# Kernel optimization log

Hardware: AMD Instinct MI355X
Metric: run time of the kernel (lower is better)

## Reference

```python
import jax, jax.numpy as jnp
import numpy as np

N = 1_000_000
C = 32
DIMS = (480, 360, 32)  # cylindrical voxel grid (z/rho, phi, height)
EPS = 1e-5


def setup_inputs() -> dict:
    rng = np.random.default_rng(0)
    total = DIMS[0] * DIMS[1] * DIMS[2]
    # unique active voxels, sorted so searchsorted gives row indices directly
    ids = np.sort(rng.choice(total, size=N, replace=False)).astype(np.int64)
    z = ids // (DIMS[1] * DIMS[2])
    rem = ids % (DIMS[1] * DIMS[2])
    y = rem // DIMS[2]
    x = rem % DIMS[2]
    coords = np.stack([z, y, x], axis=1)
    strides = np.array([DIMS[1] * DIMS[2], DIMS[2], 1], dtype=np.int64)

    def nbr(delta):
        out = np.full((3, N), -1, dtype=np.int32)
        for a in range(3):
            tgt = ids + delta * strides[a]
            ok = (coords[:, a] + delta >= 0) & (coords[:, a] + delta < DIMS[a])
            pos = np.searchsorted(ids, tgt)
            pos_c = np.clip(pos, 0, N - 1)
            found = ok & (ids[pos_c] == tgt)
            out[a] = np.where(found, pos_c, -1).astype(np.int32)
        return out

    nbr_prev = nbr(-1)
    nbr_next = nbr(+1)

    key = jax.random.key(0)
    k0, k1, k2 = jax.random.split(key, 3)
    features = jax.random.normal(k0, (N, C), dtype=jnp.float32)
    # W[branch, tap, in, out]; taps ordered (-1, 0, +1) along the branch's axis
    W = jax.random.normal(k1, (3, 3, C, C), dtype=jnp.float32) * (1.0 / np.sqrt(3 * C))
    gamma = jnp.ones((3, C), dtype=jnp.float32)
    beta = jnp.zeros((3, C), dtype=jnp.float32)
    mean = jax.random.normal(k2, (3, C), dtype=jnp.float32) * 0.1
    var = jnp.ones((3, C), dtype=jnp.float32)
    return {
        "features": features,
        "nbr_prev": jnp.asarray(nbr_prev),
        "nbr_next": jnp.asarray(nbr_next),
        "W": W,
        "gamma": gamma,
        "beta": beta,
        "mean": mean,
        "var": var,
    }


def _branch(f, Wb, prev, nxt, g, b, m, v):
    # 3-tap submanifold conv along one axis: gather prev/next active neighbors
    pm = prev >= 0
    nm = nxt >= 0
    fp = jnp.where(pm[:, None], f[jnp.where(pm, prev, 0)], 0.0)
    fn = jnp.where(nm[:, None], f[jnp.where(nm, nxt, 0)], 0.0)
    out = fp @ Wb[0] + f @ Wb[1] + fn @ Wb[2]
    # BatchNorm1d (inference stats) + Sigmoid
    out = (out - m) * (g * jax.lax.rsqrt(v + EPS)) + b
    return jax.nn.sigmoid(out)


def reference(features, nbr_prev, nbr_next, W, gamma, beta, mean, var):
    acc = jnp.zeros_like(features)
    for a in range(3):  # conv3x1x1, conv1x3x1, conv1x1x3
        acc = acc + _branch(features, W[a], nbr_prev[a], nbr_next[a],
                            gamma[a], beta[a], mean[a], var[a])
    return acc * features  # sparse_add then gating with input features
```

## Files before the change

### kernel.cpp

```cpp
#include <hip/hip_runtime.h>
#include <hip/hip_bf16.h>
#include <stdint.h>


typedef __attribute__((ext_vector_type(8))) __bf16 bf16x8;
typedef __attribute__((ext_vector_type(8))) unsigned short u16x8;
typedef __attribute__((ext_vector_type(4))) float f32x4;
typedef __attribute__((ext_vector_type(2))) float f32x2;

constexpr int NVOX    = 1000000;
constexpr int NTILES  = NVOX / 16;
constexpr int TPW     = 8;
constexpr int WPB     = 4;
constexpr int NWAVES  = (NTILES + TPW - 1) / TPW;
constexpr int NBLOCKS = (NWAVES + WPB - 1) / WPB;

__device__ __forceinline__ unsigned short f2bf_rn(float f) {
    union { float f; unsigned int u; } c; c.f = f;
    return (unsigned short)((c.u + 0x8000u) >> 16);
}

__device__ __forceinline__ bf16x8 cvt_frag(f32x4 lo, f32x4 hi) {
    u16x8 r;
    #pragma unroll
    for (int i = 0; i < 4; ++i) {
        r[i]     = f2bf_rn(lo[i]);
        r[i + 4] = f2bf_rn(hi[i]);
    }
    return __builtin_bit_cast(bf16x8, r);
}

__global__ __launch_bounds__(256) void recon_kernel(
    const float* __restrict__ feat,
    const int*   __restrict__ nprev,
    const int*   __restrict__ nnext,
    const float* __restrict__ Wt,
    const float* __restrict__ gma,
    const float* __restrict__ bta,
    const float* __restrict__ mea,
    const float* __restrict__ var,
    float*       __restrict__ out)
{
    const int lane = threadIdx.x & 63;
    const int n    = lane & 15;
    const int quad = lane >> 4;

    int b   = blockIdx.x;
    int per = NBLOCKS / 8;
    int bs  = (b < per * 8) ? ((b & 7) * per + (b >> 3)) : b;
    int wv  = bs * WPB + (threadIdx.x >> 6);

    const int t0 = wv * TPW;
    if (t0 >= NTILES) return;

    bf16x8 Bf[3][3][2];
    #pragma unroll
    for (int br = 0; br < 3; ++br)
        #pragma unroll
        for (int t = 0; t < 3; ++t)
            #pragma unroll
            for (int h = 0; h < 2; ++h) {
                u16x8 tmp;
                #pragma unroll
                for (int j = 0; j < 8; ++j) {
                    int k = quad * 8 + j;
                    tmp[j] = f2bf_rn(Wt[((br * 3 + t) * 32 + k) * 32 + 2 * n + h]);
                }
                Bf[br][t][h] = __builtin_bit_cast(bf16x8, tmp);
            }

    float sc[3][2], mn[3][2], bt[3][2];
    #pragma unroll
    for (int br = 0; br < 3; ++br)
        #pragma unroll
        for (int h = 0; h < 2; ++h) {
            int c = 2 * n + h;
            float g = gma[br * 32 + c];
            float v = var[br * 32 + c];
            sc[br][h] = g * __frsqrt_rn(v + 1e-5f);
            mn[br][h] = mea[br * 32 + c];
            bt[br][h] = bta[br * 32 + c];
        }

    int ip[3], inx[3];
    {
        int row0 = t0 * 16 + n;
        #pragma unroll
        for (int a = 0; a < 3; ++a) {
            ip[a]  = nprev[a * NVOX + row0];
            inx[a] = nnext[a * NVOX + row0];
        }
    }

    #pragma unroll 1
    for (int tt = 0; tt < TPW; ++tt) {
        int tile = t0 + tt;
        if (tile >= NTILES) return;
        int base = tile * 16;
        int row  = base + n;

        const f32x4* ps = (const f32x4*)(feat + row * 32 + quad * 8);
        f32x4 s_lo = ps[0], s_hi = ps[1];
        f32x4 p_lo[3], p_hi[3], n_lo[3], n_hi[3];
        #pragma unroll
        for (int a = 0; a < 3; ++a) {
            p_lo[a] = (f32x4){0.f, 0.f, 0.f, 0.f}; p_hi[a] = p_lo[a];
            n_lo[a] = p_lo[a];                     n_hi[a] = p_lo[a];
            if (ip[a] >= 0) {
                const f32x4* pp = (const f32x4*)(feat + ip[a] * 32 + quad * 8);
                p_lo[a] = pp[0]; p_hi[a] = pp[1];
            }
            if (inx[a] >= 0) {
                const f32x4* pn = (const f32x4*)(feat + inx[a] * 32 + quad * 8);
                n_lo[a] = pn[0]; n_hi[a] = pn[1];
            }
        }

        int ipn[3], inn[3];
        if (tt + 1 < TPW && tile + 1 < NTILES) {
            int nrow = row + 16;
            #pragma unroll
            for (int a = 0; a < 3; ++a) {
                ipn[a] = nprev[a * NVOX + nrow];
                inn[a] = nnext[a * NVOX + nrow];
            }
        } else {
            #pragma unroll
            for (int a = 0; a < 3; ++a) { ipn[a] = -1; inn[a] = -1; }
        }

        bf16x8 Aself = cvt_frag(s_lo, s_hi);
        bf16x8 Ap[3], An[3];
        #pragma unroll
        for (int a = 0; a < 3; ++a) {
            Ap[a] = cvt_frag(p_lo[a], p_hi[a]);
            An[a] = cvt_frag(n_lo[a], n_hi[a]);
        }

        f32x4 acc0 = {0.f, 0.f, 0.f, 0.f}, acc1 = {0.f, 0.f, 0.f, 0.f};
        #pragma unroll
        for (int br = 0; br < 3; ++br) {
            f32x4 c0 = {0.f, 0.f, 0.f, 0.f}, c1 = {0.f, 0.f, 0.f, 0.f};
            c0 = __builtin_amdgcn_mfma_f32_16x16x32_bf16(Ap[br], Bf[br][0][0], c0, 0, 0, 0);
            c1 = __builtin_amdgcn_mfma_f32_16x16x32_bf16(Ap[br], Bf[br][0][1], c1, 0, 0, 0);
            c0 = __builtin_amdgcn_mfma_f32_16x16x32_bf16(Aself,  Bf[br][1][0], c0, 0, 0, 0);
            c1 = __builtin_amdgcn_mfma_f32_16x16x32_bf16(Aself,  Bf[br][1][1], c1, 0, 0, 0);
            c0 = __builtin_amdgcn_mfma_f32_16x16x32_bf16(An[br], Bf[br][2][0], c0, 0, 0, 0);
            c1 = __builtin_amdgcn_mfma_f32_16x16x32_bf16(An[br], Bf[br][2][1], c1, 0, 0, 0);
            #pragma unroll
            for (int r = 0; r < 4; ++r) {
                float y0 = (c0[r] - mn[br][0]) * sc[br][0] + bt[br][0];
                float y1 = (c1[r] - mn[br][1]) * sc[br][1] + bt[br][1];
                acc0[r] += __builtin_amdgcn_rcpf(1.0f + __expf(-y0));
                acc1[r] += __builtin_amdgcn_rcpf(1.0f + __expf(-y1));
            }
        }

        #pragma unroll
        for (int r = 0; r < 4; ++r) {
            int vrow = base + quad * 4 + r;
            f32x2 fv = *(const f32x2*)(feat + vrow * 32 + 2 * n);
            f32x2 ov = { acc0[r] * fv[0], acc1[r] * fv[1] };
            *(f32x2*)(out + vrow * 32 + 2 * n) = ov;
        }

        #pragma unroll
        for (int a = 0; a < 3; ++a) { ip[a] = ipn[a]; inx[a] = inn[a]; }
    }
}

extern "C" void kernel_launch(void* const* d_in, const int* in_sizes, int n_in,
                              void* d_out, int out_size, void* d_ws, size_t ws_size,
                              hipStream_t stream) {
    const float* feat  = (const float*)d_in[0];
    const int*   nprev = (const int*)d_in[1];
    const int*   nnext = (const int*)d_in[2];
    const float* Wt    = (const float*)d_in[3];
    const float* gma   = (const float*)d_in[4];
    const float* bta   = (const float*)d_in[5];
    const float* mea   = (const float*)d_in[6];
    const float* var   = (const float*)d_in[7];
    float*       o     = (float*)d_out;

    recon_kernel<<<NBLOCKS, 256, 0, stream>>>(feat, nprev, nnext, Wt,
                                              gma, bta, mea, var, o);
}
```

Baseline: 325.9 us.

## Precompute bf16 weight fragments and folded BN constants in a prep kernel

```diff
diff --git a/kernel.cpp b/kernel.cpp
--- a/kernel.cpp
+++ b/kernel.cpp
@@ -1,5 +1,4 @@
 #include <hip/hip_runtime.h>
-#include <hip/hip_bf16.h>
 #include <stdint.h>
 
 
@@ -10,36 +9,59 @@
 
 constexpr int NVOX    = 1000000;
 constexpr int NTILES  = NVOX / 16;
-constexpr int TPW     = 8;
+constexpr int TPW     = 2;
 constexpr int WPB     = 4;
 constexpr int NWAVES  = (NTILES + TPW - 1) / TPW;
 constexpr int NBLOCKS = (NWAVES + WPB - 1) / WPB;
+constexpr float LOG2E = 1.4426950408889634f;
 
-__device__ __forceinline__ unsigned short f2bf_rn(float f) {
-    union { float f; unsigned int u; } c; c.f = f;
-    return (unsigned short)((c.u + 0x8000u) >> 16);
+constexpr int WS_WELEMS = 18 * 64 * 8;
+
+__global__ __launch_bounds__(256) void prep_kernel(
+    const float* __restrict__ Wt,
+    const float* __restrict__ gma, const float* __restrict__ bta,
+    const float* __restrict__ mea, const float* __restrict__ var,
+    unsigned short* __restrict__ wsW, float* __restrict__ wsA,
+    float* __restrict__ wsB)
+{
+    int tid = blockIdx.x * 256 + threadIdx.x;
+    if (tid < WS_WELEMS) {
+        int f    = tid >> 9;
+        int rem  = tid & 511;
+        int lane = rem >> 3;
+        int j    = rem & 7;
+        int br = f / 6, t = (f >> 1) % 3, h = f & 1;
+        int n = lane & 15, quad = lane >> 4;
+        float w = Wt[((br * 3 + t) * 32 + quad * 8 + j) * 32 + 2 * n + h];
+        union { float f; unsigned u; } c; c.f = w;
+        wsW[(f * 64 + lane) * 8 + j] = (unsigned short)((c.u + 0x8000u) >> 16);
+    } else if (tid < WS_WELEMS + 96) {
+        int i = tid - WS_WELEMS;
+        float s = gma[i] * __frsqrt_rn(var[i] + 1e-5f);
+        wsA[i] = -s * LOG2E;
+        wsB[i] = (mea[i] * s - bta[i]) * LOG2E;
+    }
 }
 
+__device__ __forceinline__ unsigned pack_bf(float a, float b) {
+    union { float f; unsigned u; } ca, cb; ca.f = a; cb.f = b;
+    return __builtin_amdgcn_perm(cb.u + 0x8000u, ca.u + 0x8000u, 0x07060302u);
+}
 __device__ __forceinline__ bf16x8 cvt_frag(f32x4 lo, f32x4 hi) {
-    u16x8 r;
-    #pragma unroll
-    for (int i = 0; i < 4; ++i) {
-        r[i]     = f2bf_rn(lo[i]);
-        r[i + 4] = f2bf_rn(hi[i]);
-    }
-    return __builtin_bit_cast(bf16x8, r);
+    union { unsigned u[4]; bf16x8 v; } r;
+    r.u[0] = pack_bf(lo[0], lo[1]); r.u[1] = pack_bf(lo[2], lo[3]);
+    r.u[2] = pack_bf(hi[0], hi[1]); r.u[3] = pack_bf(hi[2], hi[3]);
+    return r.v;
 }
 
 __global__ __launch_bounds__(256) void recon_kernel(
-    const float* __restrict__ feat,
-    const int*   __restrict__ nprev,
-    const int*   __restrict__ nnext,
-    const float* __restrict__ Wt,
-    const float* __restrict__ gma,
-    const float* __restrict__ bta,
-    const float* __restrict__ mea,
-    const float* __restrict__ var,
-    float*       __restrict__ out)
+    const float*          __restrict__ feat,
+    const int*            __restrict__ nprev,
+    const int*            __restrict__ nnext,
+    const unsigned short* __restrict__ wsW,
+    const float*          __restrict__ wsA,
+    const float*          __restrict__ wsB,
+    float*                __restrict__ out)
 {
     const int lane = threadIdx.x & 63;
     const int n    = lane & 15;
@@ -53,34 +75,17 @@
     const int t0 = wv * TPW;
     if (t0 >= NTILES) return;
 
-    bf16x8 Bf[3][3][2];
+    bf16x8 Bf[18];
     #pragma unroll
-    for (int br = 0; br < 3; ++br)
-        #pragma unroll
-        for (int t = 0; t < 3; ++t)
-            #pragma unroll
-            for (int h = 0; h < 2; ++h) {
-                u16x8 tmp;
-                #pragma unroll
-                for (int j = 0; j < 8; ++j) {
-                    int k = quad * 8 + j;
-                    tmp[j] = f2bf_rn(Wt[((br * 3 + t) * 32 + k) * 32 + 2 * n + h]);
-                }
-                Bf[br][t][h] = __builtin_bit_cast(bf16x8, tmp);
-            }
+    for (int f = 0; f < 18; ++f)
+        Bf[f] = __builtin_bit_cast(bf16x8, *(const u16x8*)(wsW + (f * 64 + lane) * 8));
 
-    float sc[3][2], mn[3][2], bt[3][2];
+    f32x2 A_[3], B_[3];
     #pragma unroll
-    for (int br = 0; br < 3; ++br)
-        #pragma unroll
-        for (int h = 0; h < 2; ++h) {
-            int c = 2 * n + h;
-            float g = gma[br * 32 + c];
-            float v = var[br * 32 + c];
-            sc[br][h] = g * __frsqrt_rn(v + 1e-5f);
-            mn[br][h] = mea[br * 32 + c];
-            bt[br][h] = bta[br * 32 + c];
-        }
+    for (int br = 0; br < 3; ++br) {
+        A_[br] = *(const f32x2*)(wsA + br * 32 + 2 * n);
+        B_[br] = *(const f32x2*)(wsB + br * 32 + 2 * n);
+    }
 
     int ip[3], inx[3];
     {
@@ -95,7 +100,7 @@
     #pragma unroll 1
     for (int tt = 0; tt < TPW; ++tt) {
         int tile = t0 + tt;
-        if (tile >= NTILES) return;
+        if (tile >= NTILES) break;
         int base = tile * 16;
         int row  = base + n;
 
@@ -141,18 +146,19 @@
         #pragma unroll
         for (int br = 0; br < 3; ++br) {
             f32x4 c0 = {0.f, 0.f, 0.f, 0.f}, c1 = {0.f, 0.f, 0.f, 0.f};
-            c0 = __builtin_amdgcn_mfma_f32_16x16x32_bf16(Ap[br], Bf[br][0][0], c0, 0, 0, 0);
-            c1 = __builtin_amdgcn_mfma_f32_16x16x32_bf16(Ap[br], Bf[br][0][1], c1, 0, 0, 0);
-            c0 = __builtin_amdgcn_mfma_f32_16x16x32_bf16(Aself,  Bf[br][1][0], c0, 0, 0, 0);
-            c1 = __builtin_amdgcn_mfma_f32_16x16x32_bf16(Aself,  Bf[br][1][1], c1, 0, 0, 0);
-            c0 = __builtin_amdgcn_mfma_f32_16x16x32_bf16(An[br], Bf[br][2][0], c0, 0, 0, 0);
-            c1 = __builtin_amdgcn_mfma_f32_16x16x32_bf16(An[br], Bf[br][2][1], c1, 0, 0, 0);
+            c0 = __builtin_amdgcn_mfma_f32_16x16x32_bf16(Ap[br], Bf[br*6 + 0], c0, 0, 0, 0);
+            c1 = __builtin_amdgcn_mfma_f32_16x16x32_bf16(Ap[br], Bf[br*6 + 1], c1, 0, 0, 0);
+            c0 = __builtin_amdgcn_mfma_f32_16x16x32_bf16(Aself,  Bf[br*6 + 2], c0, 0, 0, 0);
+            c1 = __builtin_amdgcn_mfma_f32_16x16x32_bf16(Aself,  Bf[br*6 + 3], c1, 0, 0, 0);
+            c0 = __builtin_amdgcn_mfma_f32_16x16x32_bf16(An[br], Bf[br*6 + 4], c0, 0, 0, 0);
+            c1 = __builtin_amdgcn_mfma_f32_16x16x32_bf16(An[br], Bf[br*6 + 5], c1, 0, 0, 0);
+            float a0 = A_[br][0], b0 = B_[br][0], a1 = A_[br][1], b1 = B_[br][1];
             #pragma unroll
             for (int r = 0; r < 4; ++r) {
-                float y0 = (c0[r] - mn[br][0]) * sc[br][0] + bt[br][0];
-                float y1 = (c1[r] - mn[br][1]) * sc[br][1] + bt[br][1];
-                acc0[r] += __builtin_amdgcn_rcpf(1.0f + __expf(-y0));
-                acc1[r] += __builtin_amdgcn_rcpf(1.0f + __expf(-y1));
+                float e0 = __builtin_amdgcn_exp2f(__builtin_fmaf(c0[r], a0, b0));
+                float e1 = __builtin_amdgcn_exp2f(__builtin_fmaf(c1[r], a1, b1));
+                acc0[r] += __builtin_amdgcn_rcpf(1.0f + e0);
+                acc1[r] += __builtin_amdgcn_rcpf(1.0f + e1);
             }
         }
 
@@ -182,6 +188,12 @@
     const float* var   = (const float*)d_in[7];
     float*       o     = (float*)d_out;
 
-    recon_kernel<<<NBLOCKS, 256, 0, stream>>>(feat, nprev, nnext, Wt,
-                                              gma, bta, mea, var, o);
+    unsigned short* wsW = (unsigned short*)d_ws;
+    float*          wsA = (float*)((char*)d_ws + WS_WELEMS * 2);
+    float*          wsB = wsA + 96;
+
+    prep_kernel<<<(WS_WELEMS + 96 + 255) / 256, 256, 0, stream>>>(
+        Wt, gma, bta, mea, var, wsW, wsA, wsB);
+    recon_kernel<<<NBLOCKS, 256, 0, stream>>>(feat, nprev, nnext,
+                                              wsW, wsA, wsB, o);
 }
```

After: 317.0 us. 1.03x faster.
